# Optimization experiments

Hardware: AMD Instinct MI355X
Metric: run time of the kernel (lower is better)

## Reference

```python
import jax, jax.numpy as jnp
import numpy as np

# dims
N, NPG, E, D, ED = 32768, 256, 262144, 128, 32   # nodes, nodes/graph, edges, hidden, edge_dim
HG, CG = 4, 32                                    # GAT heads, per-head channels (HG*CG == D)
HA = 8                                            # global attention heads
DH = D // HA


def _glorot(key, shape):
    fan_in, fan_out = shape[0], shape[-1]
    lim = (6.0 / (fan_in + fan_out)) ** 0.5
    return jax.random.uniform(key, shape, jnp.float32, -lim, lim)


def _ln(x, g, b, eps=1e-5):
    m = x.mean(-1, keepdims=True)
    v = ((x - m) ** 2).mean(-1, keepdims=True)
    return (x - m) * jax.lax.rsqrt(v + eps) * g + b


def setup_inputs() -> dict:
    key = jax.random.key(0)
    ks = jax.random.split(key, 32)
    x = jax.random.normal(ks[0], (N, D), jnp.float32)
    src = jax.random.randint(ks[1], (E,), 0, N, jnp.int32)
    # keep edges intra-graph (graphs are contiguous blocks of NPG nodes)
    dst = (src // NPG) * NPG + jax.random.randint(ks[2], (E,), 0, NPG, jnp.int32)
    edge_index = jnp.stack([src, dst])
    edge_attr = jax.random.normal(ks[3], (E, ED), jnp.float32)
    batch = (jnp.arange(N, dtype=jnp.int32) // NPG)
    return {
        "x": x, "edge_attr": edge_attr,
        # EdgeAwareGATv2 params
        "W_src": _glorot(ks[4], (D, HG * CG)), "W_dst": _glorot(ks[5], (D, HG * CG)),
        "W_edge": _glorot(ks[6], (ED, HG * CG)), "att": _glorot(ks[7], (1, HG, CG)),
        "gat_bias": jnp.zeros((HG * CG,), jnp.float32),
        # GraphMultiHeadAttention params
        "Wq": _glorot(ks[8], (D, D)), "bq": jnp.zeros((D,), jnp.float32),
        "Wk": _glorot(ks[9], (D, D)), "bk": jnp.zeros((D,), jnp.float32),
        "Wv": _glorot(ks[10], (D, D)), "bv": jnp.zeros((D,), jnp.float32),
        "Wo": _glorot(ks[11], (D, D)), "bo": jnp.zeros((D,), jnp.float32),
        "We": _glorot(ks[12], (ED, HA)), "be": jnp.zeros((HA,), jnp.float32),
        # block norms + FFN
        "ln1_g": jnp.ones((D,), jnp.float32), "ln1_b": jnp.zeros((D,), jnp.float32),
        "W1": _glorot(ks[13], (D, 2 * D)), "b1": jnp.zeros((2 * D,), jnp.float32),
        "W2": _glorot(ks[14], (2 * D, D)), "b2": jnp.zeros((D,), jnp.float32),
        "ln2_g": jnp.ones((D,), jnp.float32), "ln2_b": jnp.zeros((D,), jnp.float32),
        "edge_index": edge_index, "batch": batch, "nodes_per_graph": NPG,
    }


def reference(x, edge_attr, W_src, W_dst, W_edge, att, gat_bias,
              Wq, bq, Wk, bk, Wv, bv, Wo, bo, We, be,
              ln1_g, ln1_b, W1, b1, W2, b2, ln2_g, ln2_b,
              edge_index, batch, nodes_per_graph):
    n = int(nodes_per_graph)
    Nn = x.shape[0]
    G = Nn // n
    src, dst = edge_index[0], edge_index[1]

    # ---- local: EdgeAwareGATv2 (segment-softmax attention over incoming edges) ----
    xs = (x @ W_src).reshape(Nn, HG, CG)
    xd = (x @ W_dst).reshape(Nn, HG, CG)
    ef = (edge_attr @ W_edge).reshape(-1, HG, CG)
    msg = jnp.tanh(xs[src] + xd[dst] + ef)                 # [E,HG,CG]
    alpha = (msg * att).sum(-1)                            # [E,HG]
    amax = jax.ops.segment_max(alpha, dst, num_segments=Nn)
    amax = jnp.where(jnp.isfinite(amax), amax, 0.0)        # nodes w/o in-edges
    ex = jnp.exp(alpha - amax[dst])
    den = jax.ops.segment_sum(ex, dst, num_segments=Nn)
    a = ex / (den[dst] + 1e-16)
    h_local = jax.ops.segment_sum(xs[src] * a[:, :, None], dst, num_segments=Nn)
    h_local = h_local.reshape(Nn, HG * CG) + gat_bias

    # ---- global: GraphMultiHeadAttention with edge bias (dense per graph) ----
    q = (x @ Wq + bq).reshape(G, n, HA, DH)
    k = (x @ Wk + bk).reshape(G, n, HA, DH)
    v = (x @ Wv + bv).reshape(G, n, HA, DH)
    attn = jnp.einsum('gnhd,gmhd->gnmh', q, k) * (DH ** -0.5)
    eb = edge_attr @ We + be                               # [E,HA]
    g_id = src // n
    intra = (g_id == dst // n)[:, None]
    attn = attn.at[g_id, src % n, dst % n].add(jnp.where(intra, eb, 0.0))
    attn = jax.nn.softmax(attn, axis=2)                    # softmax over keys (torch dim=1)
    h_attn = jnp.einsum('gnmh,gmhd->gnhd', attn, v).reshape(Nn, D)
    h_attn = h_attn @ Wo + bo

    # ---- GPS combine: residual + norm + FFN ----
    h = _ln(x + h_local + h_attn, ln1_g, ln1_b)
    ffn = jax.nn.gelu(h @ W1 + b1, approximate=False) @ W2 + b2
    return _ln(h + ffn, ln2_g, ln2_b)
```

## Files before the change

kernel.cpp:

```cpp
#include <hip/hip_runtime.h>
#include <hip/hip_bf16.h>

typedef __hip_bfloat16 bf16;
typedef __hip_bfloat162 bf162;
typedef __attribute__((ext_vector_type(8))) short short8;
typedef __attribute__((ext_vector_type(4))) float f32x4;
typedef __attribute__((ext_vector_type(16))) float f32x16;

constexpr int kN   = 32768;
constexpr int kG   = 128;
constexpr int kE   = 262144;
constexpr int kHA  = 8;

__device__ __forceinline__ float b2f(bf16 v){ return __bfloat162float(v); }
__device__ __forceinline__ bf16  f2b(float v){ return __float2bfloat16(v); }
__device__ __forceinline__ float b2f_raw(unsigned short u){
  return __uint_as_float((unsigned)u << 16);
}
__device__ __forceinline__ float tanh_fast(float x){
  float e = __expf(2.f*x);
  return 1.f - 2.f/(e+1.f);
}
__device__ __forceinline__ unsigned int cvtpk_bf16(float lo, float hi){
  unsigned int r;
  asm volatile("v_cvt_pk_bf16_f32 %0, %1, %2" : "=v"(r) : "v"(lo), "v"(hi));
  return r;
}
__device__ __forceinline__ void plane_swap(unsigned int &a, unsigned int &b){
  asm volatile("v_permlane32_swap_b32 %0, %1" : "+v"(a), "+v"(b));
}

__global__ void detect_k(const void* xraw, int* flag){
  const bf16* p = (const bf16*)xraw;
  int good = 0;
  for (int i = threadIdx.x; i < 4096; i += 256){
    float v = fabsf(b2f(p[i]));
    if (v > 0.0009765625f && v < 16.f) good++;
  }
  __shared__ int s[256];
  s[threadIdx.x] = good;
  __syncthreads();
  for (int d = 128; d; d >>= 1){
    if (threadIdx.x < d) s[threadIdx.x] += s[threadIdx.x + d];
    __syncthreads();
  }
  if (threadIdx.x == 0) *flag = (s[0] < 3500) ? 1 : 0;
}

struct ImpEnt { const void* src; void* dst; int n; };
struct ImpArgs { ImpEnt e[23]; };
__global__ __launch_bounds__(256) void import_k(ImpArgs a, const int* __restrict__ flag){
  ImpEnt en = a.e[blockIdx.y];
  const bool f32 = (*flag != 0);
  for (int i = blockIdx.x*256 + threadIdx.x; i < en.n; i += gridDim.x*256){
    float v = f32 ? ((const float*)en.src)[i] : b2f(((const bf16*)en.src)[i]);
    ((float*)en.dst)[i] = v;
  }
}

__global__ __launch_bounds__(256) void repack5_k(const float* __restrict__ W0,
    const float* __restrict__ W1p, const float* __restrict__ W2p,
    const float* __restrict__ W3p, const float* __restrict__ W4p,
    bf16* __restrict__ dst){
  int idx = blockIdx.x*256 + threadIdx.x;
  const float* Ws[5] = {W0, W1p, W2p, W3p, W4p};
  int o = idx >> 14;
  int rem = idx & 16383;
  int j = rem & 7, l = (rem >> 3) & 63, t = rem >> 9;
  int ks = t >> 3, cb = t & 7;
  int k = ks*32 + (l>>4)*8 + j;
  int c = cb*16 + (l&15);
  dst[idx] = f2b(Ws[o][k*128 + c]);
}

struct RepEnt { const float* src; bf16* dst; int total; int ncb_log; int dout; int mode; };
__global__ __launch_bounds__(256) void repack_k(RepEnt e0, RepEnt e1, RepEnt e2,
                                                RepEnt e3, RepEnt e4){
  RepEnt en = (blockIdx.y == 0) ? e0 : (blockIdx.y == 1) ? e1 :
              (blockIdx.y == 2) ? e2 : (blockIdx.y == 3) ? e3 : e4;
  int idx = blockIdx.x*256 + threadIdx.x;
  if (idx >= en.total) return;
  int j = idx & 7, l = (idx >> 3) & 63, t = idx >> 9;
  if (en.mode == 2){
    int k = (l>>4)*8 + j;
    int c = l & 15;
    en.dst[idx] = (c < 8) ? f2b(en.src[k*8 + c]) : f2b(0.f);
    return;
  }
  int ncbm = (1 << en.ncb_log) - 1;
  int ks = t >> en.ncb_log, cb = t & ncbm;
  int k = ks*32 + (l>>4)*8 + j;
  int c = cb*16 + (l&15);
  if (en.mode == 1) c = ((c & 15) << 3) | (c >> 4);
  en.dst[idx] = f2b(en.src[k*en.dout + c]);
}

__global__ __launch_bounds__(256) void gemm5_k(const void* __restrict__ xraw,
    const int* __restrict__ flag,
    const bf16* __restrict__ Wrep, const float* __restrict__ bias5,
    bf16* __restrict__ proj5){
  const int tid = threadIdx.x;
  const int wid = tid >> 6, l = tid & 63;
  const long r0 = (long)blockIdx.x*64 + wid*16;
  const bool f32 = (*flag != 0);
  short8 af[4];
  if (f32){
    const float* fr = (const float*)xraw + (r0 + (l&15))*128;
    #pragma unroll
    for (int ks=0; ks<4; ks++){
      float4 a = *(const float4*)(fr + ks*32 + (l>>4)*8);
      float4 b = *(const float4*)(fr + ks*32 + (l>>4)*8 + 4);
      union{ unsigned int u[4]; short8 s; } c;
      c.u[0]=cvtpk_bf16(a.x,a.y); c.u[1]=cvtpk_bf16(a.z,a.w);
      c.u[2]=cvtpk_bf16(b.x,b.y); c.u[3]=cvtpk_bf16(b.z,b.w);
      af[ks] = c.s;
    }
  } else {
    const short* Arow = (const short*)xraw + (r0 + (l&15))*128;
    #pragma unroll
    for (int ks=0; ks<4; ks++)
      af[ks] = *(const short8*)(Arow + ks*32 + (l>>4)*8);
  }
  const short8* Wp = (const short8*)Wrep;
  const int cc = l & 15, rr = (l >> 4) * 4;
  #pragma unroll 1
  for (int o=0; o<5; o++){
    f32x4 acc[8];
    #pragma unroll
    for (int cb=0; cb<8; cb++) acc[cb] = (f32x4){0.f,0.f,0.f,0.f};
    #pragma unroll
    for (int ks=0; ks<4; ks++){
      #pragma unroll
      for (int cb=0; cb<8; cb++){
        short8 bf = Wp[(o*32 + ks*8 + cb)*64 + l];
        acc[cb] = __builtin_amdgcn_mfma_f32_16x16x32_bf16(af[ks], bf, acc[cb], 0,0,0);
      }
    }
    bf16* outb = proj5 + (long)o*kN*128;
    #pragma unroll
    for (int cb=0; cb<8; cb++){
      float bb = bias5[o*128 + cb*16 + cc];
      #pragma unroll
      for (int r=0; r<4; r++){
        long row = r0 + rr + r;
        outb[row*128 + cb*16 + cc] = f2b(acc[cb][r] + bb);
      }
    }
  }
}

template<int DIN, int DOUT, int EPI>
__global__ __launch_bounds__(256) void gemm_mfma_k(const bf16* __restrict__ A,
    const bf16* __restrict__ Wrep, const float* __restrict__ bias,
    bf16* __restrict__ C){
  constexpr int KS = DIN/32, NCB = DOUT/16;
  const int tid = threadIdx.x;
  const int wid = tid >> 6, l = tid & 63;
  const long r0 = (long)blockIdx.x*64 + wid*16;
  const short* Arow = (const short*)(A + (r0 + (l&15))*(long)DIN);
  short8 af[KS];
  #pragma unroll
  for (int ks=0; ks<KS; ks++)
    af[ks] = *(const short8*)(Arow + ks*32 + (l>>4)*8);
  f32x4 acc[NCB];
  #pragma unroll
  for (int cb=0; cb<NCB; cb++) acc[cb] = (f32x4){0.f,0.f,0.f,0.f};
  const short8* Wp = (const short8*)Wrep;
  #pragma unroll
  for (int ks=0; ks<KS; ks++){
    #pragma unroll
    for (int cb=0; cb<NCB; cb++){
      short8 bf = Wp[(ks*NCB + cb)*64 + l];
      acc[cb] = __builtin_amdgcn_mfma_f32_16x16x32_bf16(af[ks], bf, acc[cb], 0,0,0);
    }
  }
  const int cc = l & 15, rr = (l >> 4) * 4;
  #pragma unroll
  for (int cb=0; cb<NCB; cb++){
    float bb = bias[cb*16 + cc];
    #pragma unroll
    for (int r=0; r<4; r++){
      long row = r0 + rr + r;
      float v = acc[cb][r] + bb;
      if (EPI == 2) v = 0.5f*v*(1.f + erff(v*0.70710678118654752f));
      C[row*DOUT + cb*16 + cc] = f2b(v);
    }
  }
}

__global__ void hist_k(const int* __restrict__ dstA, int* __restrict__ cnt){
  int e = blockIdx.x*256 + threadIdx.x;
  if (e < kE) atomicAdd(&cnt[dstA[e]], 1);
}

__global__ __launch_bounds__(1024) void scan_k(const int* __restrict__ cnt, int* __restrict__ rowptr){
  __shared__ int part[1024];
  const int t = threadIdx.x;
  const int base = t*32;
  int s = 0;
  #pragma unroll
  for (int i=0;i<32;i++) s += cnt[base+i];
  part[t] = s;
  __syncthreads();
  for (int d=1; d<1024; d<<=1){
    int v = (t>=d) ? part[t-d] : 0;
    __syncthreads();
    part[t] += v;
    __syncthreads();
  }
  int run = (t==0) ? 0 : part[t-1];
  for (int i=0;i<32;i++){ rowptr[base+i] = run; run += cnt[base+i]; }
  if (t == 1023) rowptr[kN] = run;
}

__global__ void scatter_k(const int* __restrict__ dstA, const int* __restrict__ rowptr,
                          int* __restrict__ cursor, int* __restrict__ eidx){
  int e = blockIdx.x*256 + threadIdx.x;
  if (e < kE){
    int d = dstA[e];
    int p = atomicAdd(&cursor[d], 1);
    eidx[rowptr[d]+p] = e;
  }
}

__global__ __launch_bounds__(256) void edge3_k(const void* __restrict__ ea_raw,
    const int* __restrict__ flag,
    const int* __restrict__ eidx, const int* __restrict__ srcA,
    const int* __restrict__ dstA,
    const bf16* __restrict__ xs, const bf16* __restrict__ xd,
    const bf16* __restrict__ WeR_edge,
    const bf16* __restrict__ WeR_eb,
    const float* __restrict__ att_f, const float* __restrict__ be_f,
    float* __restrict__ expal_t, float* __restrict__ ebuf_t,
    unsigned short* __restrict__ epack, int* __restrict__ src_t){
  __shared__ int sEid[64], sSrc[64], sDst[64];
  __shared__ float sAlphaF[64*4];
  const int tid = threadIdx.x;
  const int w = tid >> 6, l = tid & 63;
  const int p = blockIdx.x;
  const int bid = (p & 7) * (gridDim.x >> 3) + (p >> 3);
  const long t0 = (long)bid * 64;
  const bool f32 = (*flag != 0);

  if (tid < 64){
    int e = eidx[t0 + tid];
    int s = srcA[e], d = dstA[e];
    sEid[tid] = e; sSrc[tid] = s; sDst[tid] = d;
    src_t[t0 + tid] = s;
    epack[t0 + tid] = (unsigned short)(((s & 255) << 8) | (d & 255));
  }
  __syncthreads();

  short8 af;
  {
    long eoff = (long)sEid[w*16 + (l&15)]*32 + (l>>4)*8;
    if (f32){
      const float* er = (const float*)ea_raw + eoff;
      float4 a = *(const float4*)er;
      float4 b = *(const float4*)(er + 4);
      union{ unsigned int u[4]; short8 s; } c;
      c.u[0]=cvtpk_bf16(a.x,a.y); c.u[1]=cvtpk_bf16(a.z,a.w);
      c.u[2]=cvtpk_bf16(b.x,b.y); c.u[3]=cvtpk_bf16(b.z,b.w);
      af = c.s;
    } else {
      af = *(const short8*)((const short*)ea_raw + eoff);
    }
  }

  f32x4 acc[8], acc_eb;
  #pragma unroll
  for (int cb=0; cb<8; cb++){
    short8 wb = *(const short8*)((const short*)WeR_edge + (cb*64 + l)*8);
    acc[cb] = __builtin_amdgcn_mfma_f32_16x16x32_bf16(af, wb,
                (f32x4){0.f,0.f,0.f,0.f}, 0,0,0);
  }
  {
    short8 wbe = *(const short8*)((const short*)WeR_eb + l*8);
    acc_eb = __builtin_amdgcn_mfma_f32_16x16x32_bf16(af, wbe,
                (f32x4){0.f,0.f,0.f,0.f}, 0,0,0);
  }

  const int c15 = l & 15;
  const float be_v = be_f[c15 & 7];
  float4 at0 = *(const float4*)(att_f + c15*8);
  float4 at1 = *(const float4*)(att_f + c15*8 + 4);
  const float attv[8] = {at0.x,at0.y,at0.z,at0.w, at1.x,at1.y,at1.z,at1.w};
  union U8 { short8 s8; unsigned short u[8]; };
  U8 gx[4], gd[4];
  #pragma unroll
  for (int r=0; r<4; r++){
    int e_l = w*16 + (l>>4)*4 + r;
    gx[r].s8 = *(const short8*)((const short*)xs + (long)sSrc[e_l]*128 + c15*8);
    gd[r].s8 = *(const short8*)((const short*)xd + (long)sDst[e_l]*128 + c15*8);
  }
  #pragma unroll
  for (int r=0; r<4; r++){
    int e_l = w*16 + (l>>4)*4 + r;
    float hsum = 0.f;
    #pragma unroll
    for (int cb=0; cb<8; cb++){
      float v = acc[cb][r] + b2f_raw(gx[r].u[cb]) + b2f_raw(gd[r].u[cb]);
      hsum += tanh_fast(v) * attv[cb];
    }
    hsum += __shfl_xor(hsum,1);
    hsum += __shfl_xor(hsum,2);
    if ((c15 & 3) == 0) sAlphaF[e_l*4 + (c15>>2)] = __expf(hsum);
    if (c15 < 8) ebuf_t[(long)c15*kE + t0 + e_l] = acc_eb[r] + be_v;
  }
  __syncthreads();
  if (tid < 64)
    *(float4*)&expal_t[(t0 + tid)*4] = *(float4*)&sAlphaF[tid*4];
}

__global__ __launch_bounds__(256) void gat_agg_k(const float* __restrict__ expal,
    const int* __restrict__ rowptr, const int* __restrict__ src_t,
    const bf16* __restrict__ xs, const float* __restrict__ gatb_f,
    bf16* __restrict__ h_local){
  const int tid = threadIdx.x;
  const int grp = tid >> 5;
  const int l   = tid & 31;
  const int p   = blockIdx.x;
  const int bid = (p & 7) * (gridDim.x >> 3) + (p >> 3);
  const int v   = bid*8 + grp;
  const int c0  = l*4;
  const int head = l >> 3;
  const int beg = rowptr[v], end = rowptr[v+1];
  float den = 0.f, o0 = 0.f, o1 = 0.f, o2 = 0.f, o3 = 0.f;
  const unsigned short* xsu = (const unsigned short*)xs;
  for (int t = beg; t < end; t++){
    float w = expal[(long)t*4 + head];
    long s = src_t[t];
    ushort4 a = *(const ushort4*)(xsu + s*128 + c0);
    den += w;
    o0 += w*b2f_raw(a.x); o1 += w*b2f_raw(a.y);
    o2 += w*b2f_raw(a.z); o3 += w*b2f_raw(a.w);
  }
  float inv = 1.f/(den + 1e-16f);
  float4 gb = *(const float4*)(gatb_f + c0);
  unsigned int lo = cvtpk_bf16(o0*inv + gb.x, o1*inv + gb.y);
  unsigned int hi = cvtpk_bf16(o2*inv + gb.z, o3*inv + gb.w);
  *(uint2*)&((unsigned short*)h_local)[(long)v*128 + c0] = (uint2){lo, hi};
}

__global__ __launch_bounds__(512, 6) void attn2_k(const bf16* __restrict__ qb,
    const bf16* __restrict__ kb, const bf16* __restrict__ vb,
    const float* __restrict__ ebuf_t, const unsigned short* __restrict__ epack,
    const int* __restrict__ rowptr, bf16* __restrict__ hattn){
  __shared__ short Vf[16*64*8];
  __shared__ float sb[256*33];
  const int bid = blockIdx.x;
  const int h = (bid >> 3) >> 4;
  const int g = (((bid >> 3) & 15) << 3) | (bid & 7);
  const int tid = threadIdx.x;
  const int w = tid >> 6, l = tid & 63;
  const int q31 = l & 31, hi = l >> 5;
  const int nbase = g << 8;

  for (int s2 = tid; s2 < 1024; s2 += 512){
    int f = s2 >> 6, ll = s2 & 63;
    int keyb = (f>>1)*32 + (f&1)*16 + ((ll>>5)*8);
    int d = ll & 15;
    short tmp[8];
    #pragma unroll
    for (int j=0;j<8;j++)
      tmp[j] = ((const short*)vb)[((long)(nbase + keyb + j))*128 + h*16 + d];
    *(short8*)&Vf[s2*8] = *(short8*)tmp;
  }
  for (int i = tid; i < 256*33; i += 512) sb[i] = 0.f;
  short8 qf = *(const short8*)((const short*)qb + ((long)(nbase + w*32 + q31))*128 + h*16 + hi*8);
  __syncthreads();

  float lsum = 0.f;
  f32x16 oacc = {0.f,0.f,0.f,0.f,0.f,0.f,0.f,0.f,0.f,0.f,0.f,0.f,0.f,0.f,0.f,0.f};
  short8 kf = *(const short8*)((const short*)kb + ((long)(nbase + q31))*128 + h*16 + hi*8);
  #pragma unroll 1
  for (int kt = 0; kt < 8; kt++){
    int rb = rowptr[nbase + kt*32];
    int re = rowptr[nbase + kt*32 + 32];
    for (int t = rb + tid; t < re; t += 512){
      unsigned int p = epack[t];
      atomicAdd(&sb[(p>>8)*33 + (p&31)], ebuf_t[(long)h*kE + t]);
    }
    __syncthreads();
    short8 kcur = kf;
    if (kt < 7)
      kf = *(const short8*)((const short*)kb +
            ((long)(nbase + (kt+1)*32 + q31))*128 + h*16 + hi*8);
    f32x16 acc = {0.f,0.f,0.f,0.f,0.f,0.f,0.f,0.f,0.f,0.f,0.f,0.f,0.f,0.f,0.f,0.f};
    acc = __builtin_amdgcn_mfma_f32_32x32x16_bf16(kcur, qf, acc, 0, 0, 0);
    float s[16];
    float* brow = &sb[(w*32 + q31)*33];
    #pragma unroll
    for (int r=0;r<16;r++){
      int krow = (r&3) + 8*(r>>2) + 4*hi;
      s[r] = fmaf(acc[r], 0.25f, brow[krow]);
      brow[krow] = 0.f;
    }
    __syncthreads();
    float psum = 0.f;
    #pragma unroll
    for (int r=0;r<16;r++){ s[r] = __expf(s[r]); psum += s[r]; }
    lsum += psum;
    unsigned int a  = cvtpk_bf16(s[0],  s[1]);
    unsigned int b  = cvtpk_bf16(s[2],  s[3]);
    unsigned int c  = cvtpk_bf16(s[4],  s[5]);
    unsigned int d  = cvtpk_bf16(s[6],  s[7]);
    unsigned int e  = cvtpk_bf16(s[8],  s[9]);
    unsigned int f  = cvtpk_bf16(s[10], s[11]);
    unsigned int g2 = cvtpk_bf16(s[12], s[13]);
    unsigned int h2 = cvtpk_bf16(s[14], s[15]);
    plane_swap(a, c); plane_swap(b, d); plane_swap(e, g2); plane_swap(f, h2);
    union { unsigned int u[4]; short8 s8; } A1, A2;
    A1.u[0]=a; A1.u[1]=b; A1.u[2]=c; A1.u[3]=d;
    A2.u[0]=e; A2.u[1]=f; A2.u[2]=g2; A2.u[3]=h2;
    short8 v1 = *(short8*)&Vf[((kt*2+0)*64 + l)*8];
    short8 v2 = *(short8*)&Vf[((kt*2+1)*64 + l)*8];
    oacc = __builtin_amdgcn_mfma_f32_32x32x16_bf16(A1.s8, v1, oacc, 0,0,0);
    oacc = __builtin_amdgcn_mfma_f32_32x32x16_bf16(A2.s8, v2, oacc, 0,0,0);
  }
  lsum += __shfl_xor(lsum, 32);
  float linv = 1.f / lsum;
  #pragma unroll
  for (int r=0;r<16;r++){
    int qrow = (r&3) + 8*(r>>2) + 4*hi;
    float li = __shfl(linv, qrow);
    float ov = oacc[r]*li;
    if (q31 < 16)
      hattn[((long)(nbase + w*32 + qrow))*128 + h*16 + q31] = f2b(ov);
  }
}

__global__ __launch_bounds__(256) void combine_ln_k(const void* __restrict__ a,
    const bf16* __restrict__ b, const bf16* __restrict__ c3,
    const float* __restrict__ g, const float* __restrict__ bb,
    void* __restrict__ outp, const int* __restrict__ flag,
    int a_raw, int is_final){
  const int tid = threadIdx.x;
  const int lane = tid & 63;
  const long row = (long)blockIdx.x*4 + (tid>>6);
  const long base = row*128;
  float a0, a1;
  if (a_raw && (*flag)){
    const float* ap = (const float*)a;
    a0 = ap[base+lane]; a1 = ap[base+lane+64];
  } else {
    const bf16* ap = (const bf16*)a;
    a0 = b2f(ap[base+lane]); a1 = b2f(ap[base+lane+64]);
  }
  float v0 = a0 + b2f(b[base+lane]);
  float v1 = a1 + b2f(b[base+lane+64]);
  if (c3){ v0 += b2f(c3[base+lane]); v1 += b2f(c3[base+lane+64]); }
  float s = v0 + v1;
  #pragma unroll
  for (int o=1; o<64; o<<=1) s += __shfl_xor(s, o);
  float mean = s * (1.f/128.f);
  float d0 = v0 - mean, d1 = v1 - mean;
  float q = d0*d0 + d1*d1;
  #pragma unroll
  for (int o=1; o<64; o<<=1) q += __shfl_xor(q, o);
  float r = rsqrtf(q*(1.f/128.f) + 1e-5f);
  float r0v = d0*r*g[lane]    + bb[lane];
  float r1v = d1*r*g[lane+64] + bb[lane+64];
  if (is_final && (*flag)){
    float* o = (float*)outp;
    o[base+lane]    = r0v;
    o[base+lane+64] = r1v;
  } else {
    bf16* o = (bf16*)outp;
    o[base+lane]    = f2b(r0v);
    o[base+lane+64] = f2b(r1v);
  }
}

extern "C" void kernel_launch(void* const* d_in, const int* in_sizes, int n_in,
                              void* d_out, int out_size, void* d_ws, size_t ws_size,
                              hipStream_t stream){
  const void* x_raw   = d_in[0];
  const void* ea_raw  = d_in[1];
  const int*  ei      = (const int*)d_in[25];
  const int* srcA = ei;
  const int* dstA = ei + kE;

  char* ws = (char*)d_ws;
  size_t off = 0;
  auto alloc = [&](size_t bytes)->void*{
    void* p = ws + off;
    off = (off + bytes + 255) & ~(size_t)255;
    return p;
  };
  int*   flag    = (int*)alloc(4);
  float* Wsrc_f  = (float*)alloc(16384*4);
  float* Wdst_f  = (float*)alloc(16384*4);
  float* Wedge_f = (float*)alloc(4096*4);
  float* att_f   = (float*)alloc(128*4);
  float* gatb_f  = (float*)alloc(128*4);
  float* Wq_f    = (float*)alloc(16384*4);
  float* Wk_f    = (float*)alloc(16384*4);
  float* Wv_f    = (float*)alloc(16384*4);
  float* Wo_f    = (float*)alloc(16384*4);
  float* bo_f    = (float*)alloc(128*4);
  float* We_f    = (float*)alloc(256*4);
  float* be_f    = (float*)alloc(8*4);
  float* ln1g_f  = (float*)alloc(128*4);
  float* ln1b_f  = (float*)alloc(128*4);
  float* W1_f    = (float*)alloc(32768*4);
  float* b1_f    = (float*)alloc(256*4);
  float* W2_f    = (float*)alloc(32768*4);
  float* b2_f    = (float*)alloc(128*4);
  float* ln2g_f  = (float*)alloc(128*4);
  float* ln2b_f  = (float*)alloc(128*4);
  float* bias5   = (float*)alloc(640*4);
  bf16*  Wrep5   = (bf16*)alloc((size_t)5*16384*2);
  bf16*  WoR     = (bf16*)alloc((size_t)16384*2);
  bf16*  W1R     = (bf16*)alloc((size_t)32768*2);
  bf16*  W2R     = (bf16*)alloc((size_t)32768*2);
  bf16*  WeR     = (bf16*)alloc((size_t)4096*2);
  bf16*  WeRb    = (bf16*)alloc((size_t)512*2);
  bf16*  proj5   = (bf16*)alloc((size_t)5*kN*128*2);
  bf16* xs   = proj5;
  bf16* xd   = proj5 + (size_t)kN*128;
  bf16* qb   = proj5 + (size_t)2*kN*128;
  bf16* kbuf = proj5 + (size_t)3*kN*128;
  bf16* vbuf = proj5 + (size_t)4*kN*128;
  int* cnt        = (int*)alloc((size_t)2*kN*4);
  int* cursor     = cnt + kN;
  int* rowptr     = (int*)alloc((size_t)(kN+1)*4);
  int* eidx       = (int*)alloc((size_t)kE*4);
  unsigned short* epack = (unsigned short*)alloc((size_t)kE*2);
  float* ebuf_t   = (float*)alloc((size_t)8*kE*4);
  float* expal_t  = (float*)alloc((size_t)kE*4*4);
  int*   src_t    = (int*)alloc((size_t)kE*4);
  bf16* h_local   = (bf16*)alloc((size_t)kN*128*2);
  bf16* hattn_pre = (bf16*)alloc((size_t)kN*128*2);
  bf16* h_attn    = (bf16*)alloc((size_t)kN*128*2);
  bf16* hbuf      = (bf16*)alloc((size_t)kN*128*2);
  bf16* tbuf      = (bf16*)alloc((size_t)kN*256*2);
  bf16* f2buf     = (bf16*)alloc((size_t)kN*128*2);
  (void)ws_size; (void)in_sizes; (void)n_in; (void)out_size;

  dim3 b256(256);

  detect_k<<<1, b256, 0, stream>>>(x_raw, flag);
  hipMemsetAsync(bias5, 0, 256*4, stream);
  hipMemsetAsync(cnt, 0, (size_t)2*kN*4, stream);

  hist_k<<<kE/256, b256, 0, stream>>>(dstA, cnt);
  scan_k<<<1, 1024, 0, stream>>>(cnt, rowptr);
  scatter_k<<<kE/256, b256, 0, stream>>>(dstA, rowptr, cursor, eidx);

  ImpArgs ia;
  const void* srcs[23] = {d_in[2], d_in[3], d_in[4], d_in[5], d_in[6],
                          d_in[7], d_in[8], d_in[9], d_in[10], d_in[11], d_in[12],
                          d_in[13], d_in[14], d_in[15], d_in[16], d_in[17], d_in[18],
                          d_in[19], d_in[20], d_in[21], d_in[22], d_in[23], d_in[24]};
  void* dsts[23] = {Wsrc_f, Wdst_f, Wedge_f, att_f, gatb_f,
                    Wq_f, bias5+256, Wk_f, bias5+384, Wv_f, bias5+512,
                    Wo_f, bo_f, We_f, be_f, ln1g_f, ln1b_f,
                    W1_f, b1_f, W2_f, b2_f, ln2g_f, ln2b_f};
  int ns[23] = {16384, 16384, 4096, 128, 128,
                16384, 128, 16384, 128, 16384, 128,
                16384, 128, 256, 8, 128, 128,
                32768, 256, 32768, 128, 128, 128};
  for (int i=0;i<23;i++){ ia.e[i].src=srcs[i]; ia.e[i].dst=dsts[i]; ia.e[i].n=ns[i]; }
  import_k<<<dim3(64,23), b256, 0, stream>>>(ia, flag);

  repack5_k<<<(5*16384)/256, b256, 0, stream>>>(Wsrc_f, Wdst_f, Wq_f, Wk_f, Wv_f, Wrep5);
  RepEnt ro{Wo_f, WoR, 16384, 3, 128, 0};
  RepEnt r1{W1_f, W1R, 32768, 4, 256, 0};
  RepEnt r2{W2_f, W2R, 32768, 3, 128, 0};
  RepEnt re{Wedge_f, WeR, 4096, 3, 128, 1};
  RepEnt rb{We_f, WeRb, 512, 0, 8, 2};
  repack_k<<<dim3(128,5), b256, 0, stream>>>(ro, r1, r2, re, rb);

  gemm5_k<<<kN/64, b256, 0, stream>>>(x_raw, flag, Wrep5, bias5, proj5);

  edge3_k<<<kE/64, b256, 0, stream>>>(ea_raw, flag, eidx, srcA, dstA, xs, xd,
                                      WeR, WeRb, att_f, be_f,
                                      expal_t, ebuf_t, epack, src_t);

  gat_agg_k<<<kN/8, b256, 0, stream>>>(expal_t, rowptr, src_t, xs, gatb_f, h_local);

  attn2_k<<<kG*kHA, dim3(512), 0, stream>>>(qb, kbuf, vbuf, ebuf_t, epack, rowptr, hattn_pre);
  gemm_mfma_k<128,128,1><<<kN/64, b256, 0, stream>>>(hattn_pre, WoR, bo_f, h_attn);

  combine_ln_k<<<kN/4, b256, 0, stream>>>(x_raw, h_local, h_attn, ln1g_f, ln1b_f,
                                          hbuf, flag, 1, 0);

  gemm_mfma_k<128,256,2><<<kN/64, b256, 0, stream>>>(hbuf, W1R, b1_f, tbuf);
  gemm_mfma_k<256,128,1><<<kN/64, b256, 0, stream>>>(tbuf, W2R, b2_f, f2buf);

  combine_ln_k<<<kN/4, b256, 0, stream>>>(hbuf, f2buf, nullptr, ln2g_f, ln2b_f,
                                          d_out, flag, 0, 1);
}
```

Baseline: 230.5 us.

## Fuse output/FFN2 GEMMs with residual-add LayerNorm and prefetch attention edge bias

Adds a gemm_ln_k kernel that performs the 128-wide output GEMM, adds bias and residuals, and computes LayerNorm in registers with 16-lane shuffles. It replaces the Wo GEMM plus first combine_ln and the W2 GEMM plus final combine_ln. This removes two launches and the write and re-read of the h_attn and f2buf intermediates. Separately, attn2_k now preloads the rowptr bounds and prefetches the first edge-bias element of the next key tile, which should hide some global-load latency behind the MFMA work. The cost is higher register pressure in the fused kernel.

```diff
diff --git a/kernel.cpp b/kernel.cpp
--- a/kernel.cpp
+++ b/kernel.cpp
@@ -184,6 +184,82 @@
       float v = acc[cb][r] + bb;
       if (EPI == 2) v = 0.5f*v*(1.f + erff(v*0.70710678118654752f));
       C[row*DOUT + cb*16 + cc] = f2b(v);
+    }
+  }
+}
+
+template<int DIN, int FINAL>
+__global__ __launch_bounds__(256) void gemm_ln_k(const bf16* __restrict__ A,
+    const bf16* __restrict__ Wrep, const float* __restrict__ bias,
+    const bf16* __restrict__ res1, const void* __restrict__ res2raw,
+    const float* __restrict__ g, const float* __restrict__ bb,
+    void* __restrict__ outp, const int* __restrict__ flag){
+  constexpr int KS = DIN/32;
+  const int tid = threadIdx.x;
+  const int wid = tid >> 6, l = tid & 63;
+  const long r0 = (long)blockIdx.x*64 + wid*16;
+  const short* Arow = (const short*)(A + (r0 + (l&15))*(long)DIN);
+  short8 af[KS];
+  #pragma unroll
+  for (int ks=0; ks<KS; ks++)
+    af[ks] = *(const short8*)(Arow + ks*32 + (l>>4)*8);
+  f32x4 acc[8];
+  #pragma unroll
+  for (int cb=0; cb<8; cb++) acc[cb] = (f32x4){0.f,0.f,0.f,0.f};
+  const short8* Wp = (const short8*)Wrep;
+  #pragma unroll
+  for (int ks=0; ks<KS; ks++){
+    #pragma unroll
+    for (int cb=0; cb<8; cb++){
+      short8 bf = Wp[(ks*8 + cb)*64 + l];
+      acc[cb] = __builtin_amdgcn_mfma_f32_16x16x32_bf16(af[ks], bf, acc[cb], 0,0,0);
+    }
+  }
+  const int cc = l & 15, rr = (l >> 4) * 4;
+  const bool f32 = (*flag != 0);
+  float v[8][4];
+  #pragma unroll
+  for (int cb=0; cb<8; cb++){
+    float bv = bias[cb*16 + cc];
+    #pragma unroll
+    for (int r=0; r<4; r++){
+      long row = r0 + rr + r;
+      float t = acc[cb][r] + bv + b2f(res1[row*128 + cb*16 + cc]);
+      if (res2raw){
+        t += f32 ? ((const float*)res2raw)[row*128 + cb*16 + cc]
+                 : b2f(((const bf16*)res2raw)[row*128 + cb*16 + cc]);
+      }
+      v[cb][r] = t;
+    }
+  }
+  float gv[8], bbv[8];
+  #pragma unroll
+  for (int cb=0; cb<8; cb++){ gv[cb] = g[cb*16+cc]; bbv[cb] = bb[cb*16+cc]; }
+  #pragma unroll
+  for (int r=0; r<4; r++){
+    float s = 0.f;
+    #pragma unroll
+    for (int cb=0; cb<8; cb++) s += v[cb][r];
+    s += __shfl_xor(s,1); s += __shfl_xor(s,2);
+    s += __shfl_xor(s,4); s += __shfl_xor(s,8);
+    float mean = s * (1.f/128.f);
+    float q = 0.f;
+    #pragma unroll
+    for (int cb=0; cb<8; cb++){ float d = v[cb][r]-mean; q += d*d; }
+    q += __shfl_xor(q,1); q += __shfl_xor(q,2);
+    q += __shfl_xor(q,4); q += __shfl_xor(q,8);
+    float rstd = rsqrtf(q*(1.f/128.f) + 1e-5f);
+    long row = r0 + rr + r;
+    if (FINAL && f32){
+      float* o = (float*)outp;
+      #pragma unroll
+      for (int cb=0; cb<8; cb++)
+        o[row*128 + cb*16 + cc] = (v[cb][r]-mean)*rstd*gv[cb] + bbv[cb];
+    } else {
+      bf16* o = (bf16*)outp;
+      #pragma unroll
+      for (int cb=0; cb<8; cb++)
+        o[row*128 + cb*16 + cc] = f2b((v[cb][r]-mean)*rstd*gv[cb] + bbv[cb]);
     }
   }
 }
@@ -368,20 +444,33 @@
   }
   for (int i = tid; i < 256*33; i += 512) sb[i] = 0.f;
   short8 qf = *(const short8*)((const short*)qb + ((long)(nbase + w*32 + q31))*128 + h*16 + hi*8);
+  const float* ebh = ebuf_t + (long)h*kE;
+  int rp[9];
+  #pragma unroll
+  for (int i=0;i<9;i++) rp[i] = rowptr[nbase + i*32];
+  int tpre = rp[0] + tid;
+  bool have = tpre < rp[1];
+  unsigned int pp = 0; float pb = 0.f;
+  if (have){ pp = epack[tpre]; pb = ebh[tpre]; }
+  short8 kf = *(const short8*)((const short*)kb + ((long)(nbase + q31))*128 + h*16 + hi*8);
   __syncthreads();
 
   float lsum = 0.f;
   f32x16 oacc = {0.f,0.f,0.f,0.f,0.f,0.f,0.f,0.f,0.f,0.f,0.f,0.f,0.f,0.f,0.f,0.f};
-  short8 kf = *(const short8*)((const short*)kb + ((long)(nbase + q31))*128 + h*16 + hi*8);
   #pragma unroll 1
   for (int kt = 0; kt < 8; kt++){
-    int rb = rowptr[nbase + kt*32];
-    int re = rowptr[nbase + kt*32 + 32];
-    for (int t = rb + tid; t < re; t += 512){
-      unsigned int p = epack[t];
-      atomicAdd(&sb[(p>>8)*33 + (p&31)], ebuf_t[(long)h*kE + t]);
+    if (have) atomicAdd(&sb[(pp>>8)*33 + (pp&31)], pb);
+    for (int t2 = rp[kt] + tid + 512; t2 < rp[kt+1]; t2 += 512){
+      unsigned int p2 = epack[t2];
+      atomicAdd(&sb[(p2>>8)*33 + (p2&31)], ebh[t2]);
     }
     __syncthreads();
+    if (kt < 7){
+      int tn = rp[kt+1] + tid;
+      have = tn < rp[kt+2];
+      pp = 0; pb = 0.f;
+      if (have){ pp = epack[tn]; pb = ebh[tn]; }
+    } else have = false;
     short8 kcur = kf;
     if (kt < 7)
       kf = *(const short8*)((const short*)kb +
@@ -427,48 +516,6 @@
     float ov = oacc[r]*li;
     if (q31 < 16)
       hattn[((long)(nbase + w*32 + qrow))*128 + h*16 + q31] = f2b(ov);
-  }
-}
-
-__global__ __launch_bounds__(256) void combine_ln_k(const void* __restrict__ a,
-    const bf16* __restrict__ b, const bf16* __restrict__ c3,
-    const float* __restrict__ g, const float* __restrict__ bb,
-    void* __restrict__ outp, const int* __restrict__ flag,
-    int a_raw, int is_final){
-  const int tid = threadIdx.x;
-  const int lane = tid & 63;
-  const long row = (long)blockIdx.x*4 + (tid>>6);
-  const long base = row*128;
-  float a0, a1;
-  if (a_raw && (*flag)){
-    const float* ap = (const float*)a;
-    a0 = ap[base+lane]; a1 = ap[base+lane+64];
-  } else {
-    const bf16* ap = (const bf16*)a;
-    a0 = b2f(ap[base+lane]); a1 = b2f(ap[base+lane+64]);
-  }
-  float v0 = a0 + b2f(b[base+lane]);
-  float v1 = a1 + b2f(b[base+lane+64]);
-  if (c3){ v0 += b2f(c3[base+lane]); v1 += b2f(c3[base+lane+64]); }
-  float s = v0 + v1;
-  #pragma unroll
-  for (int o=1; o<64; o<<=1) s += __shfl_xor(s, o);
-  float mean = s * (1.f/128.f);
-  float d0 = v0 - mean, d1 = v1 - mean;
-  float q = d0*d0 + d1*d1;
-  #pragma unroll
-  for (int o=1; o<64; o<<=1) q += __shfl_xor(q, o);
-  float r = rsqrtf(q*(1.f/128.f) + 1e-5f);
-  float r0v = d0*r*g[lane]    + bb[lane];
-  float r1v = d1*r*g[lane+64] + bb[lane+64];
-  if (is_final && (*flag)){
-    float* o = (float*)outp;
-    o[base+lane]    = r0v;
-    o[base+lane+64] = r1v;
-  } else {
-    bf16* o = (bf16*)outp;
-    o[base+lane]    = f2b(r0v);
-    o[base+lane+64] = f2b(r1v);
   }
 }
 
@@ -532,10 +579,8 @@
   int*   src_t    = (int*)alloc((size_t)kE*4);
   bf16* h_local   = (bf16*)alloc((size_t)kN*128*2);
   bf16* hattn_pre = (bf16*)alloc((size_t)kN*128*2);
-  bf16* h_attn    = (bf16*)alloc((size_t)kN*128*2);
   bf16* hbuf      = (bf16*)alloc((size_t)kN*128*2);
   bf16* tbuf      = (bf16*)alloc((size_t)kN*256*2);
-  bf16* f2buf     = (bf16*)alloc((size_t)kN*128*2);
   (void)ws_size; (void)in_sizes; (void)n_in; (void)out_size;
 
   dim3 b256(256);
@@ -581,14 +626,14 @@
   gat_agg_k<<<kN/8, b256, 0, stream>>>(expal_t, rowptr, src_t, xs, gatb_f, h_local);
 
   attn2_k<<<kG*kHA, dim3(512), 0, stream>>>(qb, kbuf, vbuf, ebuf_t, epack, rowptr, hattn_pre);
-  gemm_mfma_k<128,128,1><<<kN/64, b256, 0, stream>>>(hattn_pre, WoR, bo_f, h_attn);
-
-  combine_ln_k<<<kN/4, b256, 0, stream>>>(x_raw, h_local, h_attn, ln1g_f, ln1b_f,
-                                          hbuf, flag, 1, 0);
+
+  gemm_ln_k<128,0><<<kN/64, b256, 0, stream>>>(hattn_pre, WoR, bo_f,
+                                               h_local, x_raw, ln1g_f, ln1b_f,
+                                               hbuf, flag);
 
   gemm_mfma_k<128,256,2><<<kN/64, b256, 0, stream>>>(hbuf, W1R, b1_f, tbuf);
-  gemm_mfma_k<256,128,1><<<kN/64, b256, 0, stream>>>(tbuf, W2R, b2_f, f2buf);
-
-  combine_ln_k<<<kN/4, b256, 0, stream>>>(hbuf, f2buf, nullptr, ln2g_f, ln2b_f,
-                                          d_out, flag, 0, 1);
-}
+
+  gemm_ln_k<256,1><<<kN/64, b256, 0, stream>>>(tbuf, W2R, b2_f,
+                                               hbuf, nullptr, ln2g_f, ln2b_f,
+                                               d_out, flag);
+}
```

Result: faster. 225.6 us (-2.1%).
